# Kernel tuning notes

Hardware: AMD Instinct MI355X
Metric: run time of the kernel (lower is better)

The kernel has to match this reference:

```python
import jax, jax.numpy as jnp
import numpy as np
from jax import lax

B, CIN, COUT, H, W, K = 8, 256, 256, 64, 64, 3
KK = K * K
PAD, STRIDE = 1, 1
EPS = 1e-5


def setup_inputs() -> dict:
    key = jax.random.key(0)
    k0, k1, k2 = jax.random.split(key, 3)
    x = jax.random.normal(k0, (B, CIN, H, W), jnp.float32)
    # offset/mask predicting conv: 3*K*K output channels (o1, o2, mask)
    w_off = jax.random.normal(k1, (3 * KK, CIN, K, K), jnp.float32) * 0.01
    b_off = jnp.zeros((3 * KK,), jnp.float32)
    # main deformable conv weight
    weight = jax.random.normal(k2, (COUT, CIN, K, K), jnp.float32) / np.sqrt(CIN * KK).astype(np.float32)
    bias = jnp.zeros((COUT,), jnp.float32)
    gamma = jnp.ones((COUT,), jnp.float32)
    beta = jnp.zeros((COUT,), jnp.float32)
    return {"x": x, "w_off": w_off, "b_off": b_off, "weight": weight,
            "bias": bias, "gamma": gamma, "beta": beta}


def _bilinear_sample(img, ph, pw):
    """img: [C,H,W]; ph,pw: [KK,H,W] float sample positions. Zero outside. -> [C,KK,H,W]"""
    h0 = jnp.floor(ph).astype(jnp.int32)
    w0 = jnp.floor(pw).astype(jnp.int32)
    h1, w1 = h0 + 1, w0 + 1
    lh = ph - h0.astype(ph.dtype)
    lw = pw - w0.astype(pw.dtype)
    hh, hw = 1.0 - lh, 1.0 - lw

    def corner(hi, wi):
        valid = (hi >= 0) & (hi < H) & (wi >= 0) & (wi < W)
        hc = jnp.clip(hi, 0, H - 1)
        wc = jnp.clip(wi, 0, W - 1)
        v = img[:, hc, wc]  # [C,KK,H,W]
        return v * valid.astype(img.dtype)[None]

    return (corner(h0, w0) * (hh * hw)[None] + corner(h0, w1) * (hh * lw)[None]
            + corner(h1, w0) * (lh * hw)[None] + corner(h1, w1) * (lh * lw)[None])


def _forward(x, w_off, b_off, weight, bias, gamma, beta):
    dn = ('NCHW', 'OIHW', 'NCHW')
    # offset/mask branch (standard conv)
    om = lax.conv_general_dilated(x, w_off, (STRIDE, STRIDE), ((PAD, PAD), (PAD, PAD)),
                                  dimension_numbers=dn) + b_off[None, :, None, None]
    o1, o2, m = jnp.split(om, 3, axis=1)
    offset = jnp.concatenate([o1, o2], axis=1)          # [B, 2*KK, H, W]
    off_h = offset[:, 0::2]                             # [B, KK, H, W] dy per tap
    off_w = offset[:, 1::2]                             # [B, KK, H, W] dx per tap
    mask = jax.nn.sigmoid(m)                            # [B, KK, H, W]

    taps = jnp.arange(KK)
    base_h = (taps // K - PAD).astype(jnp.float32)[:, None, None] \
        + (jnp.arange(H, dtype=jnp.float32) * STRIDE)[None, :, None]  # [KK,H,1]
    base_w = (taps % K - PAD).astype(jnp.float32)[:, None, None] \
        + (jnp.arange(W, dtype=jnp.float32) * STRIDE)[None, None, :]  # [KK,1,W]
    ph = base_h[None] + off_h                           # [B,KK,H,W]
    pw = base_w[None] + off_w

    sampled = jax.vmap(_bilinear_sample)(x, ph, pw)     # [B,CIN,KK,H,W]
    sampled = sampled * mask[:, None]                   # modulated (DCNv2)

    y = jnp.einsum('bckhw,ock->bohw', sampled, weight.reshape(COUT, CIN, KK))
    y = y + bias[None, :, None, None]

    # BatchNorm2d (training mode: batch statistics) + ReLU
    mean = y.mean(axis=(0, 2, 3))
    var = y.var(axis=(0, 2, 3))
    yn = (y - mean[None, :, None, None]) * lax.rsqrt(var + EPS)[None, :, None, None]
    out = jax.nn.relu(gamma[None, :, None, None] * yn + beta[None, :, None, None])
    return out


def reference(x, w_off, b_off, weight, bias, gamma, beta):
    return _forward(x, w_off, b_off, weight, bias, gamma, beta)
```

## Files before the change

### kernel.cpp

```cpp
#include <hip/hip_runtime.h>
#include <cstdint>

#define BB    8
#define CIN   256
#define COUT  256
#define HH    64
#define WW    64
#define HWSZ  4096
#define NPIX  32768
#define NTAP  9

typedef __attribute__((ext_vector_type(8))) short    s16x8;
typedef __attribute__((ext_vector_type(8))) unsigned short u16x8;
typedef __attribute__((ext_vector_type(4))) unsigned short u16x4;
typedef __attribute__((ext_vector_type(4))) float    f32x4;

__device__ __forceinline__ float bf2f(unsigned short u) {
    unsigned int v = ((unsigned int)u) << 16;
    return __builtin_bit_cast(float, v);
}
__device__ __forceinline__ unsigned short f2bf(float f) {
    unsigned int u = __builtin_bit_cast(unsigned int, f);
    unsigned int r = (u + 0x7FFFu + ((u >> 16) & 1u)) >> 16;
    return (unsigned short)r;
}

__global__ void k_pack_x(const float* __restrict__ x, unsigned short* __restrict__ xT) {
    int blk = blockIdx.x;
    int c0 = (blk & 3) * 64;
    int h  = (blk >> 2) & 63;
    int b  = blk >> 8;
    __shared__ float tile[64][65];
    int t = threadIdx.x;
#pragma unroll
    for (int r = 0; r < 16; ++r) {
        int idx = t + r * 256;
        int i = idx >> 6, w = idx & 63;
        tile[i][w] = x[(((b * 256 + c0 + i) * 64 + h) * 64) + w];
    }
    __syncthreads();
#pragma unroll
    for (int r = 0; r < 16; ++r) {
        int idx = t + r * 256;
        int w = idx >> 6, c = idx & 63;
        xT[((b * 64 + h) * 64 + w) * 256 + c0 + c] = f2bf(tile[c][w]);
    }
}

__global__ void k_pack_wk(const float* __restrict__ w, unsigned short* __restrict__ wT) {
    int idx = blockIdx.x * 256 + threadIdx.x;
    int j   = idx & 7;
    int q   = (idx >> 3) & 3;
    int o16 = (idx >> 5) & 15;
    int n16 = (idx >> 9) & 15;
    int kc  = (idx >> 13) & 7;
    int tp  = idx >> 16;
    int c = kc * 32 + q * 8 + j;
    int o = n16 * 16 + o16;
    wT[idx] = f2bf(w[(o * 256 + c) * 9 + tp]);
}

__global__ void k_pack_woff(const float* __restrict__ w, unsigned short* __restrict__ wT) {
    int idx = blockIdx.x * 256 + threadIdx.x;
    int c  = idx & 255;
    int j  = (idx >> 8) & 31;
    int tp = idx >> 13;
    float v = (j < 27) ? w[(j * 256 + c) * 9 + tp] : 0.f;
    wT[idx] = f2bf(v);
}

__global__ __launch_bounds__(256, 2)
void k_offconv(const unsigned short* __restrict__ xT,
               const unsigned short* __restrict__ wofT,
               const float* __restrict__ b_off,
               float* __restrict__ om) {
    int blk = blockIdx.x;
    int b = blk >> 6, h = blk & 63;
    int P0 = blk * 64;
    int t = threadIdx.x;
    int lane = t & 63, wv = t >> 6;
    int p0w = wv * 16;
    int lm = lane & 15, q = lane >> 4;
    __shared__ unsigned short S3[3 * 66 * 136];

    const f32x4 FZ = {0.f, 0.f, 0.f, 0.f};
    f32x4 acc0 = FZ, acc1 = FZ;

    for (int cc = 0; cc < 2; ++cc) {
        __syncthreads();
        if (t < 96) {
            int rr = t >> 5, col = (t >> 4) & 1, c8 = (t & 15) * 8;
            u16x8 z = {0,0,0,0,0,0,0,0};
            *reinterpret_cast<u16x8*>(&S3[(rr * 66 + col * 65) * 136 + c8]) = z;
        }
#pragma unroll
        for (int r = 0; r < 12; ++r) {
            int v = t + r * 256;
            int rr = v >> 10, rem = v & 1023;
            int w = rem >> 4, c8 = (rem & 15) * 8;
            int hr = h + rr - 1;
            u16x8 d = {0,0,0,0,0,0,0,0};
            if (hr >= 0 && hr < 64)
                d = *reinterpret_cast<const u16x8*>(xT + ((b * 64 + hr) * 64 + w) * 256 + cc * 128 + c8);
            *reinterpret_cast<u16x8*>(&S3[(rr * 66 + w + 1) * 136 + c8]) = d;
        }
        __syncthreads();
#pragma unroll
        for (int tp = 0; tp < 9; ++tp) {
            int dh = tp / 3, dw = tp % 3;
            const unsigned short* wb = wofT + (tp * 32 + lm) * 256 + cc * 128;
#pragma unroll
            for (int kc = 0; kc < 4; ++kc) {
                s16x8 a = *reinterpret_cast<const s16x8*>(&S3[(dh * 66 + p0w + lm + dw) * 136 + kc * 32 + q * 8]);
                s16x8 b0 = *reinterpret_cast<const s16x8*>(wb + kc * 32 + q * 8);
                s16x8 b1 = *reinterpret_cast<const s16x8*>(wb + 16 * 256 + kc * 32 + q * 8);
                acc0 = __builtin_amdgcn_mfma_f32_16x16x32_bf16(a, b0, acc0, 0, 0, 0);
                acc1 = __builtin_amdgcn_mfma_f32_16x16x32_bf16(a, b1, acc1, 0, 0, 0);
            }
        }
    }
#pragma unroll
    for (int n = 0; n < 2; ++n) {
        int j = n * 16 + lm;
        float bj = (j < 27) ? b_off[j] : 0.f;
        f32x4 a = n ? acc1 : acc0;
#pragma unroll
        for (int i = 0; i < 4; ++i) {
            int prow = p0w + q * 4 + i;
            om[(P0 + prow) * 32 + j] = a[i] + bj;
        }
    }
}

__global__ __launch_bounds__(512, 4)
void k_main(const unsigned short* __restrict__ xT,
            const unsigned short* __restrict__ wTk,
            const float* __restrict__ om,
            const float* __restrict__ bias,
            unsigned short* __restrict__ y16,
            float* __restrict__ gsum, float* __restrict__ gssq) {
    int blk = blockIdx.x;
    int b = blk >> 6, h = blk & 63;
    int P0 = blk * 64;
    int t = threadIdx.x;
    int lane = t & 63, wv = t >> 6;
    int lm = lane & 15, q = lane >> 4;
    int o0 = wv * 32;

    __shared__ unsigned short S[64 * 264];
    __shared__ float sumbuf[256];
    __shared__ float ssqbuf[256];
    if (t < 256) sumbuf[t] = 0.f; else ssqbuf[t - 256] = 0.f;

    const f32x4 FZ = {0.f, 0.f, 0.f, 0.f};
    f32x4 acc[4][2];
#pragma unroll
    for (int m = 0; m < 4; ++m)
#pragma unroll
        for (int n = 0; n < 2; ++n) acc[m][n] = FZ;

    int p  = wv * 8 + (lane >> 3);
    int s  = lane & 7;
    int P  = P0 + p;
    int rb = b * 4096;

    for (int tp = 0; tp < 9; ++tp) {
        float oh = om[P * 32 + 2 * tp];
        float ow = om[P * 32 + 2 * tp + 1];
        float mv = om[P * 32 + 18 + tp];
        float mk = 1.f / (1.f + __expf(-mv));
        float ph = (float)(h + tp / 3 - 1) + oh;
        float pw = (float)(p + tp % 3 - 1) + ow;
        float fh0 = floorf(ph), fw0 = floorf(pw);
        int ih0 = (int)fh0, iw0 = (int)fw0;
        float lh = ph - fh0, lw = pw - fw0;
        float hh = 1.f - lh, hw_ = 1.f - lw;
        bool vh0 = (ih0 >= 0) & (ih0 < 64);
        bool vh1 = (ih0 + 1 >= 0) & (ih0 + 1 < 64);
        bool vw0 = (iw0 >= 0) & (iw0 < 64);
        bool vw1 = (iw0 + 1 >= 0) & (iw0 + 1 < 64);
        float w00 = hh * hw_ * mk * (float)(vh0 & vw0);
        float w01 = hh * lw  * mk * (float)(vh0 & vw1);
        float w10 = lh * hw_ * mk * (float)(vh1 & vw0);
        float w11 = lh * lw  * mk * (float)(vh1 & vw1);
        int ch0 = min(max(ih0, 0), 63), ch1 = min(max(ih0 + 1, 0), 63);
        int cw0 = min(max(iw0, 0), 63), cw1 = min(max(iw0 + 1, 0), 63);
        int a00 = ((rb + ch0 * 64 + cw0) * 256) + s * 8;
        int a01 = ((rb + ch0 * 64 + cw1) * 256) + s * 8;
        int a10 = ((rb + ch1 * 64 + cw0) * 256) + s * 8;
        int a11 = ((rb + ch1 * 64 + cw1) * 256) + s * 8;

        __syncthreads();
#pragma unroll
        for (int j = 0; j < 4; ++j) {
            u16x8 r00 = *reinterpret_cast<const u16x8*>(xT + a00 + j * 64);
            u16x8 r01 = *reinterpret_cast<const u16x8*>(xT + a01 + j * 64);
            u16x8 r10 = *reinterpret_cast<const u16x8*>(xT + a10 + j * 64);
            u16x8 r11 = *reinterpret_cast<const u16x8*>(xT + a11 + j * 64);
            u16x8 res;
#pragma unroll
            for (int k = 0; k < 8; ++k) {
                float v = w00 * bf2f(r00[k]);
                v = fmaf(w01, bf2f(r01[k]), v);
                v = fmaf(w10, bf2f(r10[k]), v);
                v = fmaf(w11, bf2f(r11[k]), v);
                res[k] = f2bf(v);
            }
            *reinterpret_cast<u16x8*>(&S[p * 264 + j * 64 + s * 8]) = res;
        }
        __syncthreads();

        const unsigned short* wtap = wTk + (size_t)tp * 65536 + (size_t)(wv * 2) * 512
                                   + lm * 32 + q * 8;
#pragma unroll
        for (int kc = 0; kc < 8; ++kc) {
            const unsigned short* wb = wtap + kc * 8192;
            s16x8 b0 = *reinterpret_cast<const s16x8*>(wb);
            s16x8 b1 = *reinterpret_cast<const s16x8*>(wb + 512);
#pragma unroll
            for (int mt = 0; mt < 4; ++mt) {
                s16x8 a = *reinterpret_cast<const s16x8*>(&S[(mt * 16 + lm) * 264 + kc * 32 + q * 8]);
                acc[mt][0] = __builtin_amdgcn_mfma_f32_16x16x32_bf16(a, b0, acc[mt][0], 0, 0, 0);
                acc[mt][1] = __builtin_amdgcn_mfma_f32_16x16x32_bf16(a, b1, acc[mt][1], 0, 0, 0);
            }
        }
    }

    u16x4* yv = reinterpret_cast<u16x4*>(y16);
#pragma unroll
    for (int nt = 0; nt < 2; ++nt) {
        int o = o0 + nt * 16 + lm;
        float bo = bias[o];
        float sacc = 0.f, ssacc = 0.f;
#pragma unroll
        for (int mt = 0; mt < 4; ++mt) {
            u16x4 st;
#pragma unroll
            for (int i = 0; i < 4; ++i) {
                float v = acc[mt][nt][i] + bo;
                st[i] = f2bf(v);
                sacc += v; ssacc += v * v;
            }
            int idx4 = (((blk * 8 + wv) * 2 + nt) * 4 + mt) * 64 + lane;
            yv[idx4] = st;
        }
        atomicAdd(&sumbuf[o], sacc);
        atomicAdd(&ssqbuf[o], ssacc);
    }
    __syncthreads();
    if (t < 256) atomicAdd(&gsum[t], sumbuf[t]);
    else         atomicAdd(&gssq[t - 256], ssqbuf[t - 256]);
}

__global__ void k_bnrelu(const unsigned short* __restrict__ y16,
                         const float* __restrict__ gsum, const float* __restrict__ gssq,
                         const float* __restrict__ gamma, const float* __restrict__ beta,
                         float* __restrict__ out) {
    int blk = blockIdx.x;
    int b = blk >> 6, h = blk & 63;
    __shared__ unsigned short T[64 * 257];
    __shared__ float sc[256], sh[256];
    int t = threadIdx.x;
    {
        const float n = 32768.f;
        float mean = gsum[t] / n;
        float var = gssq[t] / n - mean * mean;
        float inv = rsqrtf(var + 1e-5f);
        float s = gamma[t] * inv;
        sc[t] = s;
        sh[t] = beta[t] - mean * s;
    }
    const u16x4* yv = reinterpret_cast<const u16x4*>(y16) + blk * 4096;
#pragma unroll
    for (int r = 0; r < 16; ++r) {
        int v = t + r * 256;
        u16x4 d = yv[v];
        int lane = v & 63, mt = (v >> 6) & 3, nt = (v >> 8) & 1, wvv = (v >> 9) & 7;
        int p = mt * 16 + (lane >> 4) * 4;
        int o = wvv * 32 + nt * 16 + (lane & 15);
        T[(p + 0) * 257 + o] = d[0];
        T[(p + 1) * 257 + o] = d[1];
        T[(p + 2) * 257 + o] = d[2];
        T[(p + 3) * 257 + o] = d[3];
    }
    __syncthreads();
    int w = t & 63;
    int ob = (t >> 6) * 64;
    float* obase = out + (size_t)b * (256 * 4096) + h * 64 + w;
#pragma unroll 4
    for (int rr = 0; rr < 64; ++rr) {
        int o = ob + rr;
        float v = bf2f(T[w * 257 + o]);
        obase[(size_t)o * 4096] = fmaxf(v * sc[o] + sh[o], 0.f);
    }
}

extern "C" void kernel_launch(void* const* d_in, const int* in_sizes, int n_in,
                              void* d_out, int out_size, void* d_ws, size_t ws_size,
                              hipStream_t stream) {
    const float* x      = (const float*)d_in[0];
    const float* w_off  = (const float*)d_in[1];
    const float* b_off  = (const float*)d_in[2];
    const float* weight = (const float*)d_in[3];
    const float* bias   = (const float*)d_in[4];
    const float* gamma  = (const float*)d_in[5];
    const float* beta   = (const float*)d_in[6];

    char* ws = (char*)d_ws;
    const size_t OFF_XT    = 0;
    const size_t OFF_WT    = OFF_XT + 16777216;
    const size_t OFF_WOFT  = OFF_WT + 1179648;
    const size_t OFF_OM    = OFF_WOFT + 147456;
    const size_t OFF_Y16   = OFF_OM + 4194304;
    const size_t OFF_SUM   = OFF_Y16 + 16777216;
    const size_t OFF_SUMSQ = OFF_SUM + 1024;

    unsigned short* xT   = (unsigned short*)(ws + OFF_XT);
    unsigned short* wTk  = (unsigned short*)(ws + OFF_WT);
    unsigned short* wofT = (unsigned short*)(ws + OFF_WOFT);
    float* om    = (float*)(ws + OFF_OM);
    unsigned short* y16  = (unsigned short*)(ws + OFF_Y16);
    float* sum   = (float*)(ws + OFF_SUM);
    float* sumsq = (float*)(ws + OFF_SUMSQ);

    hipMemsetAsync(ws + OFF_SUM, 0, 2048, stream);

    k_pack_x   <<<2048, 256, 0, stream>>>(x, xT);
    k_pack_wk  <<<2304, 256, 0, stream>>>(weight, wTk);
    k_pack_woff<<< 288, 256, 0, stream>>>(w_off, wofT);
    k_offconv  <<< 512, 256, 0, stream>>>(xT, wofT, b_off, om);
    k_main     <<< 512, 512, 0, stream>>>(xT, wTk, om, bias, y16, sum, sumsq);
    k_bnrelu   <<< 512, 256, 0, stream>>>(y16, sum, sumsq, gamma, beta, (float*)d_out);
}
```

Before: 242.0 us.

## Double-buffer deformable sampling, prefetch next tap gathers, stage offsets in LDS

The main kernel now double-buffers the sampled-tile LDS and issues the next tap's bilinear gather loads before running the current tap's MFMAs, so global-load latency overlaps with matrix work and one barrier per tap goes away. Offsets and masks for the block are staged once into LDS. Block indices are remapped so consecutive blocks cover different batches. The per-block LDS stat reduction is replaced by wave shuffles followed by direct global atomics. In exchange, register pressure rises (launch bounds are lowered to 2 blocks per SM), LDS use doubles, and global atomic traffic increases.

```diff
diff --git a/kernel.cpp b/kernel.cpp
--- a/kernel.cpp
+++ b/kernel.cpp
@@ -27,9 +27,10 @@
 
 __global__ void k_pack_x(const float* __restrict__ x, unsigned short* __restrict__ xT) {
     int blk = blockIdx.x;
-    int c0 = (blk & 3) * 64;
-    int h  = (blk >> 2) & 63;
-    int b  = blk >> 8;
+    int b    = blk & 7;
+    int rest = blk >> 3;
+    int h    = rest >> 2;
+    int c0   = (rest & 3) * 64;
     __shared__ float tile[64][65];
     int t = threadIdx.x;
 #pragma unroll
@@ -75,8 +76,8 @@
                const float* __restrict__ b_off,
                float* __restrict__ om) {
     int blk = blockIdx.x;
-    int b = blk >> 6, h = blk & 63;
-    int P0 = blk * 64;
+    int b = blk & 7, h = blk >> 3;
+    int P0 = (b * 64 + h) * 64;
     int t = threadIdx.x;
     int lane = t & 63, wv = t >> 6;
     int p0w = wv * 16;
@@ -132,7 +133,7 @@
     }
 }
 
-__global__ __launch_bounds__(512, 4)
+__global__ __launch_bounds__(512, 2)
 void k_main(const unsigned short* __restrict__ xT,
             const unsigned short* __restrict__ wTk,
             const float* __restrict__ om,
@@ -140,17 +141,22 @@
             unsigned short* __restrict__ y16,
             float* __restrict__ gsum, float* __restrict__ gssq) {
     int blk = blockIdx.x;
-    int b = blk >> 6, h = blk & 63;
-    int P0 = blk * 64;
+    int b = blk & 7, h = blk >> 3;
+    int pblk = b * 64 + h;
+    int P0 = pblk * 64;
     int t = threadIdx.x;
     int lane = t & 63, wv = t >> 6;
     int lm = lane & 15, q = lane >> 4;
     int o0 = wv * 32;
 
-    __shared__ unsigned short S[64 * 264];
-    __shared__ float sumbuf[256];
-    __shared__ float ssqbuf[256];
-    if (t < 256) sumbuf[t] = 0.f; else ssqbuf[t - 256] = 0.f;
+    __shared__ unsigned short S[2][64 * 264];
+    __shared__ float OMS[64 * 32];
+
+    {
+        float4 tmp = *reinterpret_cast<const float4*>(om + P0 * 32 + t * 4);
+        *reinterpret_cast<float4*>(&OMS[t * 4]) = tmp;
+    }
+    __syncthreads();
 
     const f32x4 FZ = {0.f, 0.f, 0.f, 0.f};
     f32x4 acc[4][2];
@@ -161,13 +167,16 @@
 
     int p  = wv * 8 + (lane >> 3);
     int s  = lane & 7;
-    int P  = P0 + p;
     int rb = b * 4096;
 
-    for (int tp = 0; tp < 9; ++tp) {
-        float oh = om[P * 32 + 2 * tp];
-        float ow = om[P * 32 + 2 * tp + 1];
-        float mv = om[P * 32 + 18 + tp];
+    float w00, w01, w10, w11;
+    int a00, a01, a10, a11;
+    u16x8 r00[4], r01[4], r10[4], r11[4];
+
+    auto setup = [&](int tp) {
+        float oh = OMS[p * 32 + 2 * tp];
+        float ow = OMS[p * 32 + 2 * tp + 1];
+        float mv = OMS[p * 32 + 18 + tp];
         float mk = 1.f / (1.f + __expf(-mv));
         float ph = (float)(h + tp / 3 - 1) + oh;
         float pw = (float)(p + tp % 3 - 1) + ow;
@@ -179,36 +188,51 @@
         bool vh1 = (ih0 + 1 >= 0) & (ih0 + 1 < 64);
         bool vw0 = (iw0 >= 0) & (iw0 < 64);
         bool vw1 = (iw0 + 1 >= 0) & (iw0 + 1 < 64);
-        float w00 = hh * hw_ * mk * (float)(vh0 & vw0);
-        float w01 = hh * lw  * mk * (float)(vh0 & vw1);
-        float w10 = lh * hw_ * mk * (float)(vh1 & vw0);
-        float w11 = lh * lw  * mk * (float)(vh1 & vw1);
+        w00 = hh * hw_ * mk * (float)(vh0 & vw0);
+        w01 = hh * lw  * mk * (float)(vh0 & vw1);
+        w10 = lh * hw_ * mk * (float)(vh1 & vw0);
+        w11 = lh * lw  * mk * (float)(vh1 & vw1);
         int ch0 = min(max(ih0, 0), 63), ch1 = min(max(ih0 + 1, 0), 63);
         int cw0 = min(max(iw0, 0), 63), cw1 = min(max(iw0 + 1, 0), 63);
-        int a00 = ((rb + ch0 * 64 + cw0) * 256) + s * 8;
-        int a01 = ((rb + ch0 * 64 + cw1) * 256) + s * 8;
-        int a10 = ((rb + ch1 * 64 + cw0) * 256) + s * 8;
-        int a11 = ((rb + ch1 * 64 + cw1) * 256) + s * 8;
-
-        __syncthreads();
+        a00 = ((rb + ch0 * 64 + cw0) * 256) + s * 8;
+        a01 = ((rb + ch0 * 64 + cw1) * 256) + s * 8;
+        a10 = ((rb + ch1 * 64 + cw0) * 256) + s * 8;
+        a11 = ((rb + ch1 * 64 + cw1) * 256) + s * 8;
+    };
+    auto issue = [&]() {
 #pragma unroll
         for (int j = 0; j < 4; ++j) {
-            u16x8 r00 = *reinterpret_cast<const u16x8*>(xT + a00 + j * 64);
-            u16x8 r01 = *reinterpret_cast<const u16x8*>(xT + a01 + j * 64);
-            u16x8 r10 = *reinterpret_cast<const u16x8*>(xT + a10 + j * 64);
-            u16x8 r11 = *reinterpret_cast<const u16x8*>(xT + a11 + j * 64);
+            r00[j] = *reinterpret_cast<const u16x8*>(xT + a00 + j * 64);
+            r01[j] = *reinterpret_cast<const u16x8*>(xT + a01 + j * 64);
+            r10[j] = *reinterpret_cast<const u16x8*>(xT + a10 + j * 64);
+            r11[j] = *reinterpret_cast<const u16x8*>(xT + a11 + j * 64);
+        }
+    };
+
+    setup(0);
+    issue();
+
+    for (int tp = 0; tp < 9; ++tp) {
+        int cur = tp & 1;
+#pragma unroll
+        for (int j = 0; j < 4; ++j) {
             u16x8 res;
 #pragma unroll
             for (int k = 0; k < 8; ++k) {
-                float v = w00 * bf2f(r00[k]);
-                v = fmaf(w01, bf2f(r01[k]), v);
-                v = fmaf(w10, bf2f(r10[k]), v);
-                v = fmaf(w11, bf2f(r11[k]), v);
+                float v = w00 * bf2f(r00[j][k]);
+                v = fmaf(w01, bf2f(r01[j][k]), v);
+                v = fmaf(w10, bf2f(r10[j][k]), v);
+                v = fmaf(w11, bf2f(r11[j][k]), v);
                 res[k] = f2bf(v);
             }
-            *reinterpret_cast<u16x8*>(&S[p * 264 + j * 64 + s * 8]) = res;
+            *reinterpret_cast<u16x8*>(&S[cur][p * 264 + j * 64 + s * 8]) = res;
         }
         __syncthreads();
+
+        if (tp < 8) {
+            setup(tp + 1);
+            issue();
+        }
 
         const unsigned short* wtap = wTk + (size_t)tp * 65536 + (size_t)(wv * 2) * 512
                                    + lm * 32 + q * 8;
@@ -219,7 +243,7 @@
             s16x8 b1 = *reinterpret_cast<const s16x8*>(wb + 512);
 #pragma unroll
             for (int mt = 0; mt < 4; ++mt) {
-                s16x8 a = *reinterpret_cast<const s16x8*>(&S[(mt * 16 + lm) * 264 + kc * 32 + q * 8]);
+                s16x8 a = *reinterpret_cast<const s16x8*>(&S[cur][(mt * 16 + lm) * 264 + kc * 32 + q * 8]);
                 acc[mt][0] = __builtin_amdgcn_mfma_f32_16x16x32_bf16(a, b0, acc[mt][0], 0, 0, 0);
                 acc[mt][1] = __builtin_amdgcn_mfma_f32_16x16x32_bf16(a, b1, acc[mt][1], 0, 0, 0);
             }
@@ -241,15 +265,18 @@
                 st[i] = f2bf(v);
                 sacc += v; ssacc += v * v;
             }
-            int idx4 = (((blk * 8 + wv) * 2 + nt) * 4 + mt) * 64 + lane;
+            int idx4 = (((pblk * 8 + wv) * 2 + nt) * 4 + mt) * 64 + lane;
             yv[idx4] = st;
         }
-        atomicAdd(&sumbuf[o], sacc);
-        atomicAdd(&ssqbuf[o], ssacc);
-    }
-    __syncthreads();
-    if (t < 256) atomicAdd(&gsum[t], sumbuf[t]);
-    else         atomicAdd(&gssq[t - 256], ssqbuf[t - 256]);
+        sacc  += __shfl_xor(sacc, 16);
+        sacc  += __shfl_xor(sacc, 32);
+        ssacc += __shfl_xor(ssacc, 16);
+        ssacc += __shfl_xor(ssacc, 32);
+        if (q == 0) {
+            atomicAdd(&gsum[o], sacc);
+            atomicAdd(&gssq[o], ssacc);
+        }
+    }
 }
 
 __global__ void k_bnrelu(const unsigned short* __restrict__ y16,
@@ -257,7 +284,8 @@
                          const float* __restrict__ gamma, const float* __restrict__ beta,
                          float* __restrict__ out) {
     int blk = blockIdx.x;
-    int b = blk >> 6, h = blk & 63;
+    int b = blk & 7, h = blk >> 3;
+    int pblk = b * 64 + h;
     __shared__ unsigned short T[64 * 257];
     __shared__ float sc[256], sh[256];
     int t = threadIdx.x;
@@ -270,7 +298,7 @@
         sc[t] = s;
         sh[t] = beta[t] - mean * s;
     }
-    const u16x4* yv = reinterpret_cast<const u16x4*>(y16) + blk * 4096;
+    const u16x4* yv = reinterpret_cast<const u16x4*>(y16) + pblk * 4096;
 #pragma unroll
     for (int r = 0; r < 16; ++r) {
         int v = t + r * 256;
```

New measurement: 227.1 us. 6.2% less time.
